# Kernel optimization log

Hardware: AMD Instinct MI355X
Metric: run time of the kernel (lower is better)

The kernel has to match this reference:

```python
import jax, jax.numpy as jnp
import numpy as np

OUT_FEATURES = 8192
IN_FEATURES = 8192
BATCH = 512


def setup_inputs() -> dict:
    key = jax.random.key(0)
    k_x, k_w, k_s = jax.random.split(key, 3)
    x = jax.random.normal(k_x, (BATCH, IN_FEATURES), dtype=jnp.float32)
    # packed int4 weights: each int holds two nibbles (values 0..255)
    packed_weight = jax.random.randint(k_w, (OUT_FEATURES, IN_FEATURES // 2), 0, 256, dtype=jnp.int32)
    # per-output-row scale (positive, as produced by abs-max quantization)
    scale = jax.random.uniform(k_s, (OUT_FEATURES, 1), dtype=jnp.float32) * 0.02 + 1e-4
    return {"x": x, "packed_weight": packed_weight, "scale": scale}


def reference(x, packed_weight, scale):
    # Unpack two 4-bit values per byte: high nibble first (matches torch loop:
    # col i <- packed >> 4 & 15, col i+1 <- packed & 15), then subtract zero-point 8.
    hi = (packed_weight >> 4) & 15
    lo = packed_weight & 15
    q = jnp.stack([hi, lo], axis=-1).reshape(OUT_FEATURES, IN_FEATURES) - 8  # [out, in] int
    w = q.astype(scale.dtype) * scale  # dequantized weight [out, in]
    # linear: y = x @ W^T
    return jnp.einsum('bi,oi->bo', x, w)
```

## Files before the change

### kernel.cpp

```cpp
#include <hip/hip_runtime.h>
#include <cstdint>
#include <cstddef>

#define IN_F 8192
#define OUT_F 8192
#define BATCH 512
#define KSPLIT 4
#define KSLICE (IN_F / KSPLIT)
#define BK 64
#define NIT (KSLICE / BK)

typedef __bf16 bf16x8 __attribute__((ext_vector_type(8)));
typedef float floatx4 __attribute__((ext_vector_type(4)));

__device__ __forceinline__ ushort f2bf(float f) {
  uint32_t u = __float_as_uint(f);
  u += 0x7FFFu + ((u >> 16) & 1u);
  return (ushort)(u >> 16);
}

__device__ __forceinline__ uint32_t perm(uint32_t a, uint32_t b, uint32_t s) {
  return __builtin_amdgcn_perm(a, b, s);
}

__device__ __forceinline__ uint32_t low4(const int4 p) {
  uint32_t qa = perm((uint32_t)p.y, (uint32_t)p.x, 0x00000400u);
  uint32_t qb = perm((uint32_t)p.w, (uint32_t)p.z, 0x00000400u);
  return perm(qb, qa, 0x05040100u);
}

__device__ __forceinline__ bf16x8 unpack8(uint32_t u) {
  uint32_t hi = (u >> 4) & 0x0F0F0F0Fu;
  uint32_t lo = u & 0x0F0F0F0Fu;
  uint32_t hl0 = perm(hi, lo, 0x01050004u);
  uint32_t hl1 = perm(hi, lo, 0x03070206u);
  const uint32_t c43 = 0x43434343u;
  uint4 d;
  d.x = perm(hl0, c43, 0x00050004u);
  d.y = perm(hl0, c43, 0x00070006u);
  d.z = perm(hl1, c43, 0x00050004u);
  d.w = perm(hl1, c43, 0x00070006u);
  union { uint4 u4; bf16x8 v; } cv;
  cv.u4 = d;
  return cv.v;
}

__device__ __forceinline__ void async_copy16(const void* g, void* l) {
  __builtin_amdgcn_global_load_lds((__attribute__((address_space(1))) void*)(g),
                                   (__attribute__((address_space(3))) void*)(l),
                                   16, 0, 0);
}

__global__ __launch_bounds__(256) void cvt_rowsum(const float* __restrict__ x,
                                                  ushort* __restrict__ xb,
                                                  float* __restrict__ rowsum) {
  const int b = blockIdx.x;
  const int t = threadIdx.x;
  const float4* xr = (const float4*)(x + (size_t)b * IN_F);
  ushort4* xo = (ushort4*)(xb + (size_t)b * IN_F);
  float s[4] = {0.f, 0.f, 0.f, 0.f};
#pragma unroll
  for (int i = 0; i < 8; ++i) {
    float4 v = xr[i * 256 + t];
    ushort4 o;
    o.x = f2bf(v.x); o.y = f2bf(v.y); o.z = f2bf(v.z); o.w = f2bf(v.w);
    xo[i * 256 + t] = o;
    s[i >> 1] += __uint_as_float((uint32_t)o.x << 16) + __uint_as_float((uint32_t)o.y << 16)
               + __uint_as_float((uint32_t)o.z << 16) + __uint_as_float((uint32_t)o.w << 16);
  }
  __shared__ float red[4][4];
  const int lane = t & 63, wid = t >> 6;
#pragma unroll
  for (int j = 0; j < 4; ++j) {
    float v = s[j];
#pragma unroll
    for (int off = 32; off >= 1; off >>= 1) v += __shfl_down(v, off, 64);
    if (lane == 0) red[wid][j] = v;
  }
  __syncthreads();
  if (t < 4) rowsum[t * BATCH + b] = red[0][t] + red[1][t] + red[2][t] + red[3][t];
}

#define NPKT (OUT_F * (IN_F / 2) / 16)
__global__ __launch_bounds__(256) void bcompact(const int* __restrict__ pw,
                                                int4* __restrict__ bc) {
  const int g = blockIdx.x * 256 + threadIdx.x;
#pragma unroll
  for (int i = 0; i < 4; ++i) {
    const size_t p = (size_t)g + (size_t)i * 524288;
    const int4* src = (const int4*)(pw + p * 16);
    int4 a = src[0], b = src[1], c = src[2], d = src[3];
    int4 o;
    o.x = (int)low4(a); o.y = (int)low4(b); o.z = (int)low4(c); o.w = (int)low4(d);
    bc[p] = o;
  }
}

__global__ __launch_bounds__(256, 4) void qgemm(const ushort* __restrict__ xb,
                                                const char* __restrict__ bc,
                                                const float* __restrict__ scale,
                                                const float* __restrict__ rowsum,
                                                float* __restrict__ out) {
  __shared__ __align__(16) char Asm[2][16384];
  __shared__ __align__(16) char Bsm[2][4096];

  const int tid = threadIdx.x;
  const int lane = tid & 63;
  const int w = tid >> 6;
  const int wm = w & 1, wn = w >> 1;
  const int lr = lane & 15, lq = lane >> 4;

  const int n0 = blockIdx.x * 128;
  const int m0 = blockIdx.y * 128;
  const int ks = blockIdx.z;

  const int aRow = w * 32 + (lane >> 3);
  const int ac = ((lane & 7) ^ ((lane >> 3) & 7)) * 16;
  const char* aG = (const char*)xb + (size_t)(m0 + aRow) * (IN_F * 2) + ks * (KSLICE * 2) + ac;
  char* aL = Asm[0] + w * 4096;

  const char* bG = bc + (size_t)(n0 + (tid >> 1)) * (IN_F / 2) + ks * (KSLICE / 2) + (tid & 1) * 16;
  char* bL = Bsm[0] + w * 1024;

  floatx4 acc[4][4] = {};

  const char* aBase = Asm[0] + (wm * 64 + lr) * 128;
  const char* bBase = Bsm[0] + (wn * 64 + lr) * 32 + lq * 4;

#pragma unroll
  for (int j = 0; j < 4; ++j)
    async_copy16(aG + (size_t)j * 8 * (IN_F * 2), aL + j * 1024);
  async_copy16(bG, bL);

#pragma unroll 2
  for (int it = 0; it < NIT; ++it) {
    const int c = it & 1;
    __syncthreads();
    if (it + 1 < NIT) {
      const int nc = c ^ 1;
      const char* ag = aG + (it + 1) * (BK * 2);
#pragma unroll
      for (int j = 0; j < 4; ++j)
        async_copy16(ag + (size_t)j * 8 * (IN_F * 2), aL + nc * 16384 + j * 1024);
      async_copy16(bG + (it + 1) * (BK / 2), bL + nc * 4096);
    }
#pragma unroll
    for (int kk = 0; kk < 2; ++kk) {
      const int pc = ((kk * 4 + lq) ^ (lr & 7)) * 16;
      bf16x8 av[4], bv[4];
#pragma unroll
      for (int mi = 0; mi < 4; ++mi)
        av[mi] = *(const bf16x8*)(aBase + c * 16384 + mi * 2048 + pc);
#pragma unroll
      for (int ni = 0; ni < 4; ++ni)
        bv[ni] = unpack8(*(const uint32_t*)(bBase + c * 4096 + ni * 512 + kk * 16));
#pragma unroll
      for (int mi = 0; mi < 4; ++mi)
#pragma unroll
        for (int ni = 0; ni < 4; ++ni)
          acc[mi][ni] = __builtin_amdgcn_mfma_f32_16x16x32_bf16(av[mi], bv[ni],
                                                                acc[mi][ni], 0, 0, 0);
    }
  }

  const int om = m0 + wm * 64 + lq * 4;
  const int on = n0 + wn * 64 + lr;
  float scv[4];
#pragma unroll
  for (int ni = 0; ni < 4; ++ni) scv[ni] = scale[on + ni * 16];
  float rsv[4][4];
#pragma unroll
  for (int mi = 0; mi < 4; ++mi)
#pragma unroll
    for (int rr = 0; rr < 4; ++rr)
      rsv[mi][rr] = rowsum[ks * BATCH + om + mi * 16 + rr];

#pragma unroll
  for (int mi = 0; mi < 4; ++mi)
#pragma unroll
    for (int ni = 0; ni < 4; ++ni) {
      const float s = scv[ni];
      float* op = out + (size_t)(om + mi * 16) * OUT_F + (on + ni * 16);
#pragma unroll
      for (int rr = 0; rr < 4; ++rr)
        atomicAdd(op + (size_t)rr * OUT_F, s * (acc[mi][ni][rr] - 136.f * rsv[mi][rr]));
    }
}

extern "C" void kernel_launch(void* const* d_in, const int* in_sizes, int n_in,
                              void* d_out, int out_size, void* d_ws, size_t ws_size,
                              hipStream_t stream) {
  const float* x = (const float*)d_in[0];
  const int* pw = (const int*)d_in[1];
  const float* scale = (const float*)d_in[2];
  float* out = (float*)d_out;

  ushort* xb = (ushort*)d_ws;
  float* rowsum = (float*)((char*)d_ws + (8u << 20));
  char* bc = (char*)d_ws + (16u << 20);

  cvt_rowsum<<<BATCH, 256, 0, stream>>>(x, xb, rowsum);
  bcompact<<<2048, 256, 0, stream>>>(pw, (int4*)bc);
  hipMemsetAsync(out, 0, (size_t)out_size * sizeof(float), stream);
  dim3 grid(OUT_F / 128, BATCH / 128, KSPLIT);
  qgemm<<<grid, 256, 0, stream>>>(xb, bc, scale, rowsum, out);
}
```

Measured before the change: 312.6 us.

## Replace direct-to-LDS async copies with register-staged prefetch and swizzled B stores

```diff
diff --git a/kernel.cpp b/kernel.cpp
--- a/kernel.cpp
+++ b/kernel.cpp
@@ -45,12 +45,6 @@
   return cv.v;
 }
 
-__device__ __forceinline__ void async_copy16(const void* g, void* l) {
-  __builtin_amdgcn_global_load_lds((__attribute__((address_space(1))) void*)(g),
-                                   (__attribute__((address_space(3))) void*)(l),
-                                   16, 0, 0);
-}
-
 __global__ __launch_bounds__(256) void cvt_rowsum(const float* __restrict__ x,
                                                   ushort* __restrict__ xb,
                                                   float* __restrict__ rowsum) {
@@ -81,7 +75,6 @@
   if (t < 4) rowsum[t * BATCH + b] = red[0][t] + red[1][t] + red[2][t] + red[3][t];
 }
 
-#define NPKT (OUT_F * (IN_F / 2) / 16)
 __global__ __launch_bounds__(256) void bcompact(const int* __restrict__ pw,
                                                 int4* __restrict__ bc) {
   const int g = blockIdx.x * 256 + threadIdx.x;
@@ -96,7 +89,7 @@
   }
 }
 
-__global__ __launch_bounds__(256, 4) void qgemm(const ushort* __restrict__ xb,
+__global__ __launch_bounds__(256, 3) void qgemm(const ushort* __restrict__ xb,
                                                 const char* __restrict__ bc,
                                                 const float* __restrict__ scale,
                                                 const float* __restrict__ rowsum,
@@ -114,46 +107,53 @@
   const int m0 = blockIdx.y * 128;
   const int ks = blockIdx.z;
 
-  const int aRow = w * 32 + (lane >> 3);
-  const int ac = ((lane & 7) ^ ((lane >> 3) & 7)) * 16;
-  const char* aG = (const char*)xb + (size_t)(m0 + aRow) * (IN_F * 2) + ks * (KSLICE * 2) + ac;
-  char* aL = Asm[0] + w * 4096;
-
-  const char* bG = bc + (size_t)(n0 + (tid >> 1)) * (IN_F / 2) + ks * (KSLICE / 2) + (tid & 1) * 16;
-  char* bL = Bsm[0] + w * 1024;
+  const int r = tid >> 1, h = tid & 1;
+  const char* aG = (const char*)xb + (size_t)(m0 + r) * (IN_F * 2) + ks * (KSLICE * 2) + h * 64;
+  const char* bG = bc + (size_t)(n0 + r) * (IN_F / 2) + ks * (KSLICE / 2) + h * 16;
+
+  int aWoff[4];
+#pragma unroll
+  for (int j = 0; j < 4; ++j)
+    aWoff[j] = r * 128 + (((h * 4 + j) ^ (r & 7)) * 16);
+  const int bWoff = r * 32 + ((h ^ ((r >> 2) & 1)) * 16);
+
+  const int aRbase = (wm * 64 + lr) * 128;
+  const int bRbase = (wn * 64 + lr) * 32 + lq * 4;
+  const int bSel = (lr >> 2) & 1;
 
   floatx4 acc[4][4] = {};
 
-  const char* aBase = Asm[0] + (wm * 64 + lr) * 128;
-  const char* bBase = Bsm[0] + (wn * 64 + lr) * 32 + lq * 4;
-
-#pragma unroll
-  for (int j = 0; j < 4; ++j)
-    async_copy16(aG + (size_t)j * 8 * (IN_F * 2), aL + j * 1024);
-  async_copy16(bG, bL);
+  int4 pa[2][4];
+  int4 pb[2];
+#pragma unroll
+  for (int j = 0; j < 4; ++j) pa[0][j] = *(const int4*)(aG + j * 16);
+  pb[0] = *(const int4*)(bG);
 
 #pragma unroll 2
   for (int it = 0; it < NIT; ++it) {
-    const int c = it & 1;
+    const int c = it & 1, nc = c ^ 1;
+    if (it + 1 < NIT) {
+      const char* ag = aG + (it + 1) * (BK * 2);
+#pragma unroll
+      for (int j = 0; j < 4; ++j) pa[nc][j] = *(const int4*)(ag + j * 16);
+      pb[nc] = *(const int4*)(bG + (it + 1) * (BK / 2));
+    }
+#pragma unroll
+    for (int j = 0; j < 4; ++j)
+      *(int4*)(Asm[c] + aWoff[j]) = pa[c][j];
+    *(int4*)(Bsm[c] + bWoff) = pb[c];
     __syncthreads();
-    if (it + 1 < NIT) {
-      const int nc = c ^ 1;
-      const char* ag = aG + (it + 1) * (BK * 2);
-#pragma unroll
-      for (int j = 0; j < 4; ++j)
-        async_copy16(ag + (size_t)j * 8 * (IN_F * 2), aL + nc * 16384 + j * 1024);
-      async_copy16(bG + (it + 1) * (BK / 2), bL + nc * 4096);
-    }
 #pragma unroll
     for (int kk = 0; kk < 2; ++kk) {
+      bf16x8 av[4], bv[4];
       const int pc = ((kk * 4 + lq) ^ (lr & 7)) * 16;
-      bf16x8 av[4], bv[4];
 #pragma unroll
       for (int mi = 0; mi < 4; ++mi)
-        av[mi] = *(const bf16x8*)(aBase + c * 16384 + mi * 2048 + pc);
+        av[mi] = *(const bf16x8*)(Asm[c] + aRbase + mi * 2048 + pc);
+      const int bslot = (kk ^ bSel) * 16;
 #pragma unroll
       for (int ni = 0; ni < 4; ++ni)
-        bv[ni] = unpack8(*(const uint32_t*)(bBase + c * 4096 + ni * 512 + kk * 16));
+        bv[ni] = unpack8(*(const uint32_t*)(Bsm[c] + bRbase + ni * 512 + bslot));
 #pragma unroll
       for (int mi = 0; mi < 4; ++mi)
 #pragma unroll
```

Result: slower. 509.6 us (+63.0%).
